# Performance work log

Measured on AMD Instinct MI355X. Metric: run time of the kernel, lower is better.

The kernel has to match this reference:

```python
import jax, jax.numpy as jnp
import numpy as np

D_MODEL = 768
NUM_HEADS = 12
D_HEAD = D_MODEL // NUM_HEADS


def setup_inputs() -> dict:
    key = jax.random.key(0)
    ks = jax.random.split(key, 11)
    B, S = 1, 4096
    s = 1.0 / np.sqrt(D_MODEL)
    inp = {
        'q': jax.random.normal(ks[0], (B, S, D_MODEL), dtype=jnp.float32),
        'k': jax.random.normal(ks[1], (B, S, D_MODEL), dtype=jnp.float32),
        'v': jax.random.normal(ks[2], (B, S, D_MODEL), dtype=jnp.float32),
        'wq': jax.random.normal(ks[3], (D_MODEL, D_MODEL), dtype=jnp.float32) * s,
        'bq': jnp.zeros((D_MODEL,), dtype=jnp.float32),
        'wk': jax.random.normal(ks[4], (D_MODEL, D_MODEL), dtype=jnp.float32) * s,
        'bk': jnp.zeros((D_MODEL,), dtype=jnp.float32),
        'wv': jax.random.normal(ks[5], (D_MODEL, D_MODEL), dtype=jnp.float32) * s,
        'bv': jnp.zeros((D_MODEL,), dtype=jnp.float32),
        'wo': jax.random.normal(ks[6], (D_MODEL, D_MODEL), dtype=jnp.float32) * s,
        'bo': jnp.zeros((D_MODEL,), dtype=jnp.float32),
    }
    return inp


def reference(q, k, v, wq, bq, wk, bk, wv, bv, wo, bo):
    B, S, _ = q.shape
    # linear projections (torch Linear: x @ W^T + b)
    qh = (q @ wq.T + bq).reshape(B, S, NUM_HEADS, D_HEAD).transpose(0, 2, 1, 3)
    kh = (k @ wk.T + bk).reshape(B, S, NUM_HEADS, D_HEAD).transpose(0, 2, 1, 3)
    vh = (v @ wv.T + bv).reshape(B, S, NUM_HEADS, D_HEAD).transpose(0, 2, 1, 3)
    scores = jnp.einsum('bhqd,bhkd->bhqk', qh, kh) / jnp.sqrt(jnp.float32(D_HEAD))
    causal = jnp.tril(jnp.ones((S, S), dtype=bool))  # [S,S] causal mask
    scores = jnp.where(causal, scores, jnp.finfo(scores.dtype).min)
    attn = jax.nn.softmax(scores, axis=-1)  # dropout omitted (eval mode)
    out = jnp.einsum('bhqk,bhkd->bhqd', attn, vh)
    out = out.transpose(0, 2, 1, 3).reshape(B, S, D_MODEL)
    return out @ wo.T + bo
```

## Files before the change

### kernel.cpp

```cpp
#include <hip/hip_runtime.h>
#include <stdint.h>

typedef __attribute__((ext_vector_type(8))) short short8;
typedef __attribute__((ext_vector_type(4))) short short4v;
typedef __attribute__((ext_vector_type(4))) float float4v;
typedef __attribute__((ext_vector_type(2))) uint32_t uint32x2;
typedef __attribute__((ext_vector_type(4))) uint32_t uint32x4;

__device__ __forceinline__ unsigned short f2bf(float f) {
  union { float f; uint32_t u; } v;
  v.f = f;
  uint32_t u = v.u;
  return (unsigned short)((u + 0x7fffu + ((u >> 16) & 1u)) >> 16);
}

__device__ __forceinline__ uint32_t pkbf(float a, float b) {
#if __has_builtin(__builtin_amdgcn_cvt_pk_bf16_f32)
  typedef __attribute__((ext_vector_type(2))) __bf16 bf16x2;
  bf16x2 r = __builtin_amdgcn_cvt_pk_bf16_f32(a, b);
  union { bf16x2 v; uint32_t u; } c;
  c.v = r;
  return c.u;
#else
  return (uint32_t)f2bf(a) | ((uint32_t)f2bf(b) << 16);
#endif
}

__device__ __forceinline__ float fexp2(float x) {
#if __has_builtin(__builtin_amdgcn_exp2f)
  return __builtin_amdgcn_exp2f(x);
#else
  return exp2f(x);
#endif
}

__device__ __forceinline__ float4v mfma16bf(short4v a, short4v b, float4v c) {
#if __has_builtin(__builtin_amdgcn_mfma_f32_16x16x16bf16_1k)
  return __builtin_amdgcn_mfma_f32_16x16x16bf16_1k(a, b, c, 0, 0, 0);
#else
  float4v d;
  asm("v_mfma_f32_16x16x16_bf16 %0, %1, %2, %3"
      : "=v"(d) : "v"(a), "v"(b), "v"(c));
  return d;
#endif
}

__device__ __forceinline__ void gll16(const unsigned short* g, unsigned short* l) {
  __builtin_amdgcn_global_load_lds(
      (const __attribute__((address_space(1))) void*)g,
      (__attribute__((address_space(3))) void*)l, 16, 0, 0);
}

struct CvtArgs {
  const float* src[7];
  unsigned short* dst[7];
};

__global__ __launch_bounds__(256) void cvt_all(CvtArgs a) {
  const int bid = blockIdx.x;
  int t, off;
  if (bid < 4608) { t = bid / 1536; off = bid - t * 1536; }
  else { const int b2 = bid - 4608; t = 3 + b2 / 288; off = b2 - (t - 3) * 288; }
  const size_t i = (size_t)off * 256 + threadIdx.x;
  const float4v* p = (const float4v*)(a.src[t] + i * 8);
  float4v x = p[0], y = p[1];
  uint32x4 o;
  o[0] = pkbf(x[0], x[1]);
  o[1] = pkbf(x[2], x[3]);
  o[2] = pkbf(y[0], y[1]);
  o[3] = pkbf(y[2], y[3]);
  *(uint32x4*)(a.dst[t] + i * 8) = o;
}

__global__ __launch_bounds__(256) void gemm_qkv(
    const unsigned short* __restrict__ xq, const unsigned short* __restrict__ xk,
    const unsigned short* __restrict__ xv,
    const unsigned short* __restrict__ wqb, const unsigned short* __restrict__ wkb,
    const unsigned short* __restrict__ wvb,
    const float* __restrict__ bq, const float* __restrict__ bk,
    const float* __restrict__ bv,
    unsigned short* __restrict__ Qp, unsigned short* __restrict__ Kp,
    unsigned short* __restrict__ Vt, float qscale)
{
  __shared__ unsigned short As[128 * 64];
  __shared__ unsigned short Ws[128 * 64];
  const int z = blockIdx.z;
  const unsigned short* A = z == 0 ? xq : z == 1 ? xk : xv;
  const unsigned short* W = z == 0 ? wqb : z == 1 ? wkb : wvb;
  const float* bias = z == 0 ? bq : z == 1 ? bk : bv;
  const int M = 4096, N = 768, K = 768;
  const int tid = threadIdx.x, wave = tid >> 6, lane = tid & 63;
  const int g = lane >> 4, l16 = lane & 15;
  const int sw = l16 & 7;
  const int m0 = blockIdx.x * 128, n0 = blockIdx.y * 128;
  const int wn = (wave >> 1) * 64, wm = (wave & 1) * 64;
  const int srow0 = wave * 32 + (lane >> 3);
  const int skg = lane & 7;

  float4v acc[4][4] = {};

  for (int k0 = 0; k0 < K; k0 += 64) {
    if (k0) __syncthreads();
    #pragma unroll
    for (int c = 0; c < 4; ++c) {
      const int row = srow0 + c * 8;
      const int kg = skg ^ (row & 7);
      gll16(A + (size_t)(m0 + row) * K + k0 + kg * 8, &As[(wave * 32 + c * 8) * 64]);
      gll16(W + (size_t)(n0 + row) * K + k0 + kg * 8, &Ws[(wave * 32 + c * 8) * 64]);
    }
    __syncthreads();
    #pragma unroll
    for (int kk = 0; kk < 2; ++kk) {
      const int kg = ((kk * 4 + g) ^ sw) * 8;
      short8 xf[4], wf[4];
      #pragma unroll
      for (int t = 0; t < 4; ++t) {
        xf[t] = *(const short8*)&As[(wm + t * 16 + l16) * 64 + kg];
        wf[t] = *(const short8*)&Ws[(wn + t * 16 + l16) * 64 + kg];
      }
      if (z < 2) {
        #pragma unroll
        for (int i = 0; i < 4; ++i)
          #pragma unroll
          for (int j = 0; j < 4; ++j)
            acc[i][j] = __builtin_amdgcn_mfma_f32_16x16x32_bf16(wf[i], xf[j], acc[i][j], 0, 0, 0);
      } else {
        #pragma unroll
        for (int i = 0; i < 4; ++i)
          #pragma unroll
          for (int j = 0; j < 4; ++j)
            acc[i][j] = __builtin_amdgcn_mfma_f32_16x16x32_bf16(xf[i], wf[j], acc[i][j], 0, 0, 0);
      }
    }
  }

  if (z < 2) {
    unsigned short* O = z == 0 ? Qp : Kp;
    const float osc = z == 0 ? qscale : 1.0f;
    #pragma unroll
    for (int i = 0; i < 4; ++i) {
      const int nb = n0 + wn + i * 16 + 4 * g;
      const float4v bb = *(const float4v*)&bias[nb];
      #pragma unroll
      for (int j = 0; j < 4; ++j) {
        const int m = m0 + wm + j * 16 + l16;
        uint32x2 pk;
        pk[0] = pkbf((acc[i][j][0] + bb[0]) * osc, (acc[i][j][1] + bb[1]) * osc);
        pk[1] = pkbf((acc[i][j][2] + bb[2]) * osc, (acc[i][j][3] + bb[3]) * osc);
        *(uint32x2*)(O + (size_t)m * N + nb) = pk;
      }
    }
  } else {
    #pragma unroll
    for (int j = 0; j < 4; ++j) {
      const int n = n0 + wn + j * 16 + l16;
      const float bb = bias[n];
      #pragma unroll
      for (int i = 0; i < 4; ++i) {
        const int mb = m0 + wm + i * 16 + 4 * g;
        uint32x2 pk;
        pk[0] = pkbf(acc[i][j][0] + bb, acc[i][j][1] + bb);
        pk[1] = pkbf(acc[i][j][2] + bb, acc[i][j][3] + bb);
        *(uint32x2*)(Vt + (size_t)n * M + mb) = pk;
      }
    }
  }
}

__global__ __launch_bounds__(256, 4) void flash_part(
    const unsigned short* __restrict__ Qp,
    const unsigned short* __restrict__ Kp,
    const unsigned short* __restrict__ Vt,
    unsigned short* __restrict__ Opart,
    float* __restrict__ lpart)
{
  __shared__ unsigned short lds_k[2][64 * 64];
  __shared__ unsigned short lds_v[2][64 * 64];
  const int S = 4096, DM = 768;

  const int gid = blockIdx.x;
  const int h = gid % 12;
  const int e = 79 - gid / 12;
  int t, c;
  if (e < 8)       { t = e;                c = 0; }
  else if (e < 24) { t = 8 + (e - 8) / 2;  c = (e - 8) % 2; }
  else if (e < 48) { t = 16 + (e - 24) / 3; c = (e - 24) % 3; }
  else             { t = 24 + (e - 48) / 4; c = (e - 48) % 4; }
  const int kb0 = c * 16;
  const int kbe = min(kb0 + 16, 2 * t + 2);

  const int tid = threadIdx.x, wave = tid >> 6, lane = tid & 63;
  const int g = lane >> 4, l16 = lane & 15;
  const int sw = l16 & 7;
  const int qbase = t * 128 + wave * 32;

  short8 qf[2][2];
  #pragma unroll
  for (int qc = 0; qc < 2; ++qc) {
    const unsigned short* qp = Qp + (size_t)(qbase + qc * 16 + l16) * DM + h * 64;
    qf[qc][0] = *(const short8*)(qp + g * 8);
    qf[qc][1] = *(const short8*)(qp + 32 + g * 8);
  }

  float4v o[2][4] = {};
  float lsum[2] = {0.0f, 0.0f};

  const int strow = wave * 16 + (lane >> 3);
  const int skg = lane & 7;

  #pragma unroll
  for (int cc = 0; cc < 2; ++cc) {
    const int row = strow + cc * 8;
    const int kg = skg ^ (row & 7);
    gll16(Kp + (size_t)(kb0 * 64 + row) * DM + h * 64 + kg * 8,
          &lds_k[0][(wave * 16 + cc * 8) * 64]);
    gll16(Vt + (size_t)(h * 64 + row) * S + kb0 * 64 + kg * 8,
          &lds_v[0][(wave * 16 + cc * 8) * 64]);
  }
  __syncthreads();

  for (int kb = kb0; kb < kbe; ++kb) {
    const int cur = kb & 1;
    if (kb + 1 < kbe) {
      const int nb = cur ^ 1;
      #pragma unroll
      for (int cc = 0; cc < 2; ++cc) {
        const int row = strow + cc * 8;
        const int kg = skg ^ (row & 7);
        gll16(Kp + (size_t)((kb + 1) * 64 + row) * DM + h * 64 + kg * 8,
              &lds_k[nb][(wave * 16 + cc * 8) * 64]);
        gll16(Vt + (size_t)(h * 64 + row) * S + (kb + 1) * 64 + kg * 8,
              &lds_v[nb][(wave * 16 + cc * 8) * 64]);
      }
    }
    const unsigned short* kc = lds_k[cur];
    const unsigned short* vc = lds_v[cur];

    float4v sf[2][4];
    #pragma unroll
    for (int mt = 0; mt < 4; ++mt) {
      short8 ka0 = *(const short8*)&kc[(mt * 16 + l16) * 64 + ((0 + g) ^ sw) * 8];
      short8 ka1 = *(const short8*)&kc[(mt * 16 + l16) * 64 + ((4 + g) ^ sw) * 8];
      #pragma unroll
      for (int qc = 0; qc < 2; ++qc) {
        float4v a = {};
        a = __builtin_amdgcn_mfma_f32_16x16x32_bf16(ka0, qf[qc][0], a, 0, 0, 0);
        a = __builtin_amdgcn_mfma_f32_16x16x32_bf16(ka1, qf[qc][1], a, 0, 0, 0);
        sf[qc][mt] = a;
      }
    }

    if ((kb + 1) * 64 > qbase) {
      #pragma unroll
      for (int qc = 0; qc < 2; ++qc) {
        const int q = qbase + qc * 16 + l16;
        #pragma unroll
        for (int mt = 0; mt < 4; ++mt)
          #pragma unroll
          for (int rr = 0; rr < 4; ++rr) {
            const int key = kb * 64 + mt * 16 + 4 * g + rr;
            sf[qc][mt][rr] = (key <= q) ? sf[qc][mt][rr] : -1e30f;
          }
      }
    }

    short4v pb[2][4];
    #pragma unroll
    for (int qc = 0; qc < 2; ++qc)
      #pragma unroll
      for (int mt = 0; mt < 4; ++mt) {
        float4v pe;
        #pragma unroll
        for (int rr = 0; rr < 4; ++rr) {
          pe[rr] = fexp2(sf[qc][mt][rr]);
          lsum[qc] += pe[rr];
        }
        union { uint32x2 u; short4v s; } cv;
        cv.u[0] = pkbf(pe[0], pe[1]);
        cv.u[1] = pkbf(pe[2], pe[3]);
        pb[qc][mt] = cv.s;
      }

    #pragma unroll
    for (int ms = 0; ms < 4; ++ms) {
      const int slot = ((2 * ms + (g >> 1)) ^ sw) * 8 + (g & 1) * 4;
      #pragma unroll
      for (int dt = 0; dt < 4; ++dt) {
        short4v va = *(const short4v*)&vc[(dt * 16 + l16) * 64 + slot];
        o[0][dt] = mfma16bf(va, pb[0][ms], o[0][dt]);
        o[1][dt] = mfma16bf(va, pb[1][ms], o[1][dt]);
      }
    }

    __syncthreads();
  }

  const int slot = (h * 32 + t) * 4 + c;
  unsigned short* ob = Opart + (size_t)slot * 8192;
  #pragma unroll
  for (int qc = 0; qc < 2; ++qc) {
    float L = lsum[qc];
    L += __shfl_xor(L, 16);
    L += __shfl_xor(L, 32);
    const int ql = wave * 32 + qc * 16 + l16;
    if (g == 0) lpart[slot * 128 + ql] = L;
    #pragma unroll
    for (int dt = 0; dt < 4; ++dt) {
      uint32x2 ov;
      ov[0] = pkbf(o[qc][dt][0], o[qc][dt][1]);
      ov[1] = pkbf(o[qc][dt][2], o[qc][dt][3]);
      *(uint32x2*)(ob + (size_t)ql * 64 + dt * 16 + 4 * g) = ov;
    }
  }
}

__global__ __launch_bounds__(256) void flash_combine(
    const unsigned short* __restrict__ Opart, const float* __restrict__ lpart,
    unsigned short* __restrict__ AO)
{
  const int t = blockIdx.x, h = blockIdx.y;
  const int nc = (2 * t + 17) >> 4;
  const int slot0 = (h * 32 + t) * 4;
  const int tid = threadIdx.x;
  const int qr = tid >> 2, dc = (tid & 3) * 16;
  #pragma unroll
  for (int it = 0; it < 2; ++it) {
    const int ql = it * 64 + qr;
    float acc[16];
    #pragma unroll
    for (int j = 0; j < 16; ++j) acc[j] = 0.0f;
    float lsum = 0.0f;
    for (int cc = 0; cc < nc; ++cc) {
      const int slot = slot0 + cc;
      lsum += lpart[slot * 128 + ql];
      const uint32x4* p = (const uint32x4*)(Opart + (size_t)slot * 8192 + ql * 64 + dc);
      uint32x4 w0 = p[0], w1 = p[1];
      #pragma unroll
      for (int j = 0; j < 4; ++j) {
        union { uint32_t u; float f; } lo, hi;
        lo.u = w0[j] << 16; hi.u = w0[j] & 0xffff0000u;
        acc[2 * j] += lo.f; acc[2 * j + 1] += hi.f;
        lo.u = w1[j] << 16; hi.u = w1[j] & 0xffff0000u;
        acc[8 + 2 * j] += lo.f; acc[8 + 2 * j + 1] += hi.f;
      }
    }
    const float inv = 1.0f / lsum;
    uint32x4 o0, o1;
    #pragma unroll
    for (int j = 0; j < 4; ++j) {
      o0[j] = pkbf(acc[2 * j] * inv, acc[2 * j + 1] * inv);
      o1[j] = pkbf(acc[8 + 2 * j] * inv, acc[8 + 2 * j + 1] * inv);
    }
    unsigned short* dst = AO + (size_t)(t * 128 + ql) * 768 + h * 64 + dc;
    *(uint32x4*)dst = o0;
    *(uint32x4*)(dst + 8) = o1;
  }
}

__global__ __launch_bounds__(256) void gemm_out(
    const unsigned short* __restrict__ A, const unsigned short* __restrict__ W,
    const float* __restrict__ bias, float* __restrict__ Out)
{
  __shared__ unsigned short As[128 * 64];
  __shared__ unsigned short Ws[128 * 64];
  const int N = 768, K = 768;
  const int tid = threadIdx.x, wave = tid >> 6, lane = tid & 63;
  const int g = lane >> 4, l16 = lane & 15;
  const int sw = l16 & 7;
  const int m0 = blockIdx.x * 128, n0 = blockIdx.y * 128;
  const int wn = (wave >> 1) * 64, wm = (wave & 1) * 64;
  const int srow0 = wave * 32 + (lane >> 3);
  const int skg = lane & 7;

  float4v acc[4][4] = {};

  for (int k0 = 0; k0 < K; k0 += 64) {
    if (k0) __syncthreads();
    #pragma unroll
    for (int c = 0; c < 4; ++c) {
      const int row = srow0 + c * 8;
      const int kg = skg ^ (row & 7);
      gll16(A + (size_t)(m0 + row) * K + k0 + kg * 8, &As[(wave * 32 + c * 8) * 64]);
      gll16(W + (size_t)(n0 + row) * K + k0 + kg * 8, &Ws[(wave * 32 + c * 8) * 64]);
    }
    __syncthreads();
    #pragma unroll
    for (int kk = 0; kk < 2; ++kk) {
      const int kg = ((kk * 4 + g) ^ sw) * 8;
      short8 xf[4], wf[4];
      #pragma unroll
      for (int t = 0; t < 4; ++t) {
        xf[t] = *(const short8*)&As[(wm + t * 16 + l16) * 64 + kg];
        wf[t] = *(const short8*)&Ws[(wn + t * 16 + l16) * 64 + kg];
      }
      #pragma unroll
      for (int i = 0; i < 4; ++i)
        #pragma unroll
        for (int j = 0; j < 4; ++j)
          acc[i][j] = __builtin_amdgcn_mfma_f32_16x16x32_bf16(wf[i], xf[j], acc[i][j], 0, 0, 0);
    }
  }

  #pragma unroll
  for (int i = 0; i < 4; ++i) {
    const int nb = n0 + wn + i * 16 + 4 * g;
    const float4v bb = *(const float4v*)&bias[nb];
    #pragma unroll
    for (int j = 0; j < 4; ++j) {
      const int m = m0 + wm + j * 16 + l16;
      float4v ov;
      #pragma unroll
      for (int rr = 0; rr < 4; ++rr) ov[rr] = acc[i][j][rr] + bb[rr];
      *(float4v*)(Out + (size_t)m * N + nb) = ov;
    }
  }
}

extern "C" void kernel_launch(void* const* d_in, const int* in_sizes, int n_in,
                              void* d_out, int out_size, void* d_ws, size_t ws_size,
                              hipStream_t stream) {
  const float* q  = (const float*)d_in[0];
  const float* k  = (const float*)d_in[1];
  const float* v  = (const float*)d_in[2];
  const float* wq = (const float*)d_in[3];
  const float* bq = (const float*)d_in[4];
  const float* wk = (const float*)d_in[5];
  const float* bk = (const float*)d_in[6];
  const float* wv = (const float*)d_in[7];
  const float* bv = (const float*)d_in[8];
  const float* wo = (const float*)d_in[9];
  const float* bo = (const float*)d_in[10];
  float* out = (float*)d_out;

  const int S = 4096, D = 768;
  unsigned short* Qp    = (unsigned short*)d_ws;
  unsigned short* Kp    = Qp  + (size_t)S * D;
  unsigned short* Vt    = Kp  + (size_t)S * D;
  unsigned short* AO    = Vt  + (size_t)S * D;
  unsigned short* xq    = AO  + (size_t)S * D;
  unsigned short* xk    = xq  + (size_t)S * D;
  unsigned short* xv    = xk  + (size_t)S * D;
  unsigned short* wqb   = xv  + (size_t)S * D;
  unsigned short* wkb   = wqb + (size_t)D * D;
  unsigned short* wvb   = wkb + (size_t)D * D;
  unsigned short* wob   = wvb + (size_t)D * D;
  unsigned short* Opart = wob + (size_t)D * D;
  float*          lpart = (float*)(Opart + (size_t)1536 * 8192);

  CvtArgs ca;
  ca.src[0] = q;  ca.dst[0] = xq;
  ca.src[1] = k;  ca.dst[1] = xk;
  ca.src[2] = v;  ca.dst[2] = xv;
  ca.src[3] = wq; ca.dst[3] = wqb;
  ca.src[4] = wk; ca.dst[4] = wkb;
  ca.src[5] = wv; ca.dst[5] = wvb;
  ca.src[6] = wo; ca.dst[6] = wob;

  const float SC = 0.125f * 1.44269504089f;
  dim3 blk(256);
  cvt_all<<<dim3(5760), blk, 0, stream>>>(ca);
  gemm_qkv<<<dim3(32, 6, 3), blk, 0, stream>>>(xq, xk, xv, wqb, wkb, wvb,
                                               bq, bk, bv, Qp, Kp, Vt, SC);
  flash_part<<<dim3(960), blk, 0, stream>>>(Qp, Kp, Vt, Opart, lpart);
  flash_combine<<<dim3(32, 12), blk, 0, stream>>>(Opart, lpart, AO);
  gemm_out<<<dim3(32, 6), blk, 0, stream>>>(AO, wob, bo, out);
}
```

Before: 211.2 us.

## Switch flash-attention inner loops to 32x32x16 MFMA with permlane32 swap repacking

Measured after the change: 207.1 us. Within noise of the previous version (-1.9%).

```diff
diff --git a/kernel.cpp b/kernel.cpp
--- a/kernel.cpp
+++ b/kernel.cpp
@@ -2,10 +2,11 @@
 #include <stdint.h>
 
 typedef __attribute__((ext_vector_type(8))) short short8;
-typedef __attribute__((ext_vector_type(4))) short short4v;
 typedef __attribute__((ext_vector_type(4))) float float4v;
+typedef __attribute__((ext_vector_type(16))) float f32x16;
 typedef __attribute__((ext_vector_type(2))) uint32_t uint32x2;
 typedef __attribute__((ext_vector_type(4))) uint32_t uint32x4;
+typedef __attribute__((ext_vector_type(2))) unsigned int uint2v;
 
 __device__ __forceinline__ unsigned short f2bf(float f) {
   union { float f; uint32_t u; } v;
@@ -34,14 +35,15 @@
 #endif
 }
 
-__device__ __forceinline__ float4v mfma16bf(short4v a, short4v b, float4v c) {
-#if __has_builtin(__builtin_amdgcn_mfma_f32_16x16x16bf16_1k)
-  return __builtin_amdgcn_mfma_f32_16x16x16bf16_1k(a, b, c, 0, 0, 0);
+__device__ __forceinline__ uint2v plswap(uint32_t a, uint32_t b) {
+#if __has_builtin(__builtin_amdgcn_permlane32_swap)
+  return __builtin_amdgcn_permlane32_swap(a, b, false, false);
 #else
-  float4v d;
-  asm("v_mfma_f32_16x16x16_bf16 %0, %1, %2, %3"
-      : "=v"(d) : "v"(a), "v"(b), "v"(c));
-  return d;
+  asm("v_permlane32_swap_b32 %0, %1" : "+v"(a), "+v"(b));
+  uint2v r;
+  r[0] = a;
+  r[1] = b;
+  return r;
 #endif
 }
 
@@ -190,20 +192,21 @@
   const int kbe = min(kb0 + 16, 2 * t + 2);
 
   const int tid = threadIdx.x, wave = tid >> 6, lane = tid & 63;
-  const int g = lane >> 4, l16 = lane & 15;
-  const int sw = l16 & 7;
+  const int l31 = lane & 31, hi = lane >> 5, sw7 = lane & 7;
   const int qbase = t * 128 + wave * 32;
-
-  short8 qf[2][2];
-  #pragma unroll
-  for (int qc = 0; qc < 2; ++qc) {
-    const unsigned short* qp = Qp + (size_t)(qbase + qc * 16 + l16) * DM + h * 64;
-    qf[qc][0] = *(const short8*)(qp + g * 8);
-    qf[qc][1] = *(const short8*)(qp + 32 + g * 8);
-  }
-
-  float4v o[2][4] = {};
-  float lsum[2] = {0.0f, 0.0f};
+  const int qrow = qbase + l31;
+
+  short8 qf[4];
+  {
+    const unsigned short* qp = Qp + (size_t)qrow * DM + h * 64 + hi * 8;
+    qf[0] = *(const short8*)(qp);
+    qf[1] = *(const short8*)(qp + 16);
+    qf[2] = *(const short8*)(qp + 32);
+    qf[3] = *(const short8*)(qp + 48);
+  }
+
+  f32x16 o0 = {}, o1 = {};
+  float4v ls4 = {0.f, 0.f, 0.f, 0.f};
 
   const int strow = wave * 16 + (lane >> 3);
   const int skg = lane & 7;
@@ -236,80 +239,81 @@
     const unsigned short* kc = lds_k[cur];
     const unsigned short* vc = lds_v[cur];
 
-    float4v sf[2][4];
-    #pragma unroll
-    for (int mt = 0; mt < 4; ++mt) {
-      short8 ka0 = *(const short8*)&kc[(mt * 16 + l16) * 64 + ((0 + g) ^ sw) * 8];
-      short8 ka1 = *(const short8*)&kc[(mt * 16 + l16) * 64 + ((4 + g) ^ sw) * 8];
-      #pragma unroll
-      for (int qc = 0; qc < 2; ++qc) {
-        float4v a = {};
-        a = __builtin_amdgcn_mfma_f32_16x16x32_bf16(ka0, qf[qc][0], a, 0, 0, 0);
-        a = __builtin_amdgcn_mfma_f32_16x16x32_bf16(ka1, qf[qc][1], a, 0, 0, 0);
-        sf[qc][mt] = a;
-      }
-    }
-
-    if ((kb + 1) * 64 > qbase) {
-      #pragma unroll
-      for (int qc = 0; qc < 2; ++qc) {
-        const int q = qbase + qc * 16 + l16;
+    f32x16 s0 = {}, s1 = {};
+    __builtin_amdgcn_s_setprio(1);
+    #pragma unroll
+    for (int d4 = 0; d4 < 4; ++d4) {
+      const int cg = ((2 * d4 + hi) ^ sw7) * 8;
+      short8 ka = *(const short8*)&kc[l31 * 64 + cg];
+      short8 kb2 = *(const short8*)&kc[(32 + l31) * 64 + cg];
+      s0 = __builtin_amdgcn_mfma_f32_32x32x16_bf16(ka, qf[d4], s0, 0, 0, 0);
+      s1 = __builtin_amdgcn_mfma_f32_32x32x16_bf16(kb2, qf[d4], s1, 0, 0, 0);
+    }
+    __builtin_amdgcn_s_setprio(0);
+
+    const bool diag = (kb + 1) * 64 > qbase;
+    short8 pb[4];
+    auto sm_pack = [&](const f32x16& sv, int ks, short8* pbp) {
+      #pragma unroll
+      for (int jh = 0; jh < 2; ++jh) {
+        float pe[8];
+        if (diag) {
+          #pragma unroll
+          for (int rr = 0; rr < 8; ++rr) {
+            const int key = kb * 64 + ks + (rr & 3) + 8 * (2 * jh + (rr >> 2)) + 4 * hi;
+            pe[rr] = fexp2(key <= qrow ? sv[jh * 8 + rr] : -1e30f);
+          }
+        } else {
+          #pragma unroll
+          for (int rr = 0; rr < 8; ++rr) pe[rr] = fexp2(sv[jh * 8 + rr]);
+        }
         #pragma unroll
-        for (int mt = 0; mt < 4; ++mt)
-          #pragma unroll
-          for (int rr = 0; rr < 4; ++rr) {
-            const int key = kb * 64 + mt * 16 + 4 * g + rr;
-            sf[qc][mt][rr] = (key <= q) ? sf[qc][mt][rr] : -1e30f;
-          }
-      }
-    }
-
-    short4v pb[2][4];
-    #pragma unroll
-    for (int qc = 0; qc < 2; ++qc)
-      #pragma unroll
-      for (int mt = 0; mt < 4; ++mt) {
-        float4v pe;
-        #pragma unroll
-        for (int rr = 0; rr < 4; ++rr) {
-          pe[rr] = fexp2(sf[qc][mt][rr]);
-          lsum[qc] += pe[rr];
-        }
-        union { uint32x2 u; short4v s; } cv;
-        cv.u[0] = pkbf(pe[0], pe[1]);
-        cv.u[1] = pkbf(pe[2], pe[3]);
-        pb[qc][mt] = cv.s;
-      }
-
-    #pragma unroll
-    for (int ms = 0; ms < 4; ++ms) {
-      const int slot = ((2 * ms + (g >> 1)) ^ sw) * 8 + (g & 1) * 4;
-      #pragma unroll
-      for (int dt = 0; dt < 4; ++dt) {
-        short4v va = *(const short4v*)&vc[(dt * 16 + l16) * 64 + slot];
-        o[0][dt] = mfma16bf(va, pb[0][ms], o[0][dt]);
-        o[1][dt] = mfma16bf(va, pb[1][ms], o[1][dt]);
-      }
-    }
+        for (int rr = 0; rr < 8; ++rr) ls4[rr & 3] += pe[rr];
+        const uint32_t x01 = pkbf(pe[0], pe[1]);
+        const uint32_t x23 = pkbf(pe[2], pe[3]);
+        const uint32_t y01 = pkbf(pe[4], pe[5]);
+        const uint32_t y23 = pkbf(pe[6], pe[7]);
+        uint2v r01 = plswap(x01, y01);
+        uint2v r23 = plswap(x23, y23);
+        union { uint32x4 u; short8 s; } w;
+        w.u[0] = r01[0];
+        w.u[1] = r23[0];
+        w.u[2] = r01[1];
+        w.u[3] = r23[1];
+        pbp[jh] = w.s;
+      }
+    };
+    sm_pack(s0, 0, &pb[0]);
+    sm_pack(s1, 32, &pb[2]);
+
+    __builtin_amdgcn_s_setprio(1);
+    #pragma unroll
+    for (int kk = 0; kk < 4; ++kk) {
+      const int cg = ((2 * kk + hi) ^ sw7) * 8;
+      short8 va0 = *(const short8*)&vc[l31 * 64 + cg];
+      short8 va1 = *(const short8*)&vc[(32 + l31) * 64 + cg];
+      o0 = __builtin_amdgcn_mfma_f32_32x32x16_bf16(va0, pb[kk], o0, 0, 0, 0);
+      o1 = __builtin_amdgcn_mfma_f32_32x32x16_bf16(va1, pb[kk], o1, 0, 0, 0);
+    }
+    __builtin_amdgcn_s_setprio(0);
 
     __syncthreads();
   }
 
+  float L = (ls4[0] + ls4[1]) + (ls4[2] + ls4[3]);
+  L += __shfl_xor(L, 32);
   const int slot = (h * 32 + t) * 4 + c;
-  unsigned short* ob = Opart + (size_t)slot * 8192;
+  if (hi == 0) lpart[slot * 128 + wave * 32 + l31] = L;
+  unsigned short* ob = Opart + (size_t)slot * 8192 + (size_t)(wave * 32 + l31) * 64;
   #pragma unroll
-  for (int qc = 0; qc < 2; ++qc) {
-    float L = lsum[qc];
-    L += __shfl_xor(L, 16);
-    L += __shfl_xor(L, 32);
-    const int ql = wave * 32 + qc * 16 + l16;
-    if (g == 0) lpart[slot * 128 + ql] = L;
-    #pragma unroll
-    for (int dt = 0; dt < 4; ++dt) {
+  for (int dt = 0; dt < 2; ++dt) {
+    const f32x16& oo = dt ? o1 : o0;
+    #pragma unroll
+    for (int a = 0; a < 4; ++a) {
       uint32x2 ov;
-      ov[0] = pkbf(o[qc][dt][0], o[qc][dt][1]);
-      ov[1] = pkbf(o[qc][dt][2], o[qc][dt][3]);
-      *(uint32x2*)(ob + (size_t)ql * 64 + dt * 16 + 4 * g) = ov;
+      ov[0] = pkbf(oo[4 * a + 0], oo[4 * a + 1]);
+      ov[1] = pkbf(oo[4 * a + 2], oo[4 * a + 3]);
+      *(uint32x2*)(ob + dt * 32 + 8 * a + 4 * hi) = ov;
     }
   }
 }
```
